# Kernel tuning notes

Measured on AMD Instinct MI355X. Metric: run time of the kernel, lower is better.

Reference implementation:

```python
import jax, jax.numpy as jnp
from jax import lax
import numpy as np

VAR0, VAR1 = 0.1, 0.2
K_TOP, T1, T2 = 5, 0.35, 0.5
ALPHA, GAMMA, BETA = 0.25, 2.0, 0.11


def point_form(b):
    # center form (cx,cy,w,h) -> corner form (x1,y1,x2,y2)
    return jnp.concatenate([b[:, :2] - b[:, 2:] / 2, b[:, :2] + b[:, 2:] / 2], axis=-1)


def jaccard(a, b):
    # a: [N,4], b: [P,4] corner boxes -> IoU [N,P]
    lt = jnp.maximum(a[:, None, :2], b[None, :, :2])
    rb = jnp.minimum(a[:, None, 2:], b[None, :, 2:])
    wh = jnp.clip(rb - lt, 0.0)
    inter = wh[..., 0] * wh[..., 1]
    area_a = ((a[:, 2] - a[:, 0]) * (a[:, 3] - a[:, 1]))[:, None]
    area_b = ((b[:, 2] - b[:, 0]) * (b[:, 3] - b[:, 1]))[None, :]
    return inter / (area_a + area_b - inter)


def encode(matched, priors):
    # matched: corner boxes [P,4], priors: center form [P,4]
    g_cxcy = ((matched[:, :2] + matched[:, 2:]) / 2 - priors[:, :2]) / (VAR0 * priors[:, 2:])
    g_wh = jnp.log((matched[:, 2:] - matched[:, :2]) / priors[:, 2:]) / VAR1
    return jnp.concatenate([g_cxcy, g_wh], axis=-1)


def decode(loc, priors):
    cxcy = priors[:, :2] + loc[:, :2] * VAR0 * priors[:, 2:]
    wh = priors[:, 2:] * jnp.exp(loc[:, 2:] * VAR1)
    return jnp.concatenate([cxcy - wh / 2, cxcy + wh / 2], axis=-1)


def _bce_logits(x, t):
    return jnp.maximum(x, 0.0) - x * t + jnp.log1p(jnp.exp(-jnp.abs(x)))


def focal_loss(logits, target, f_iou=None):
    C = logits.shape[-1]
    t = target.reshape(-1, 1)
    keep = (t >= 0.0).astype(logits.dtype)
    t = jnp.maximum(t, 0.0)
    pos = jnp.sum(t > 0.0).astype(logits.dtype)
    x = jnp.take_along_axis(logits.reshape(-1, C), t.astype(jnp.int32), axis=1)
    ce = _bce_logits(x, t)
    a = t * ALPHA + (1.0 - t) * (1.0 - ALPHA)
    p = jax.nn.sigmoid(x)
    pt = jnp.where(t == 1.0, p, 1.0 - p)
    if f_iou is not None:
        a = lax.stop_gradient(f_iou.reshape(-1, 1)) * a
    loss = a * (1.0 - pt) ** GAMMA * ce * keep
    return jnp.sum(loss) / jnp.maximum(pos, 1.0)


def smoothl1_masked(pred, target, mask):
    # equals SmoothL1Loss on the masked rows: sum(elem)/num_rows
    x = jnp.abs(pred - target)
    elem = jnp.where(x >= BETA, x - 0.5 * BETA, 0.5 * x * x / BETA)
    n = jnp.sum(mask).astype(pred.dtype)
    return jnp.sum(elem * mask[..., None].astype(pred.dtype)) / jnp.maximum(n, 1.0)


def match_image(loc_pred, tgt, priors_c, priors_pt):
    N = tgt.shape[0]
    P = priors_c.shape[0]
    truths = tgt[:, :4]
    labels = tgt[:, 4]
    iou = jaccard(truths, priors_pt)  # [N,P]
    bt_score = jnp.max(iou, axis=0)
    bt_idx = jnp.argmax(iou, axis=0).astype(jnp.int32)

    def greedy(_, st):
        m, s, ix = st
        flat = jnp.argmax(m)
        j = (flat // P).astype(jnp.int32)
        i = (flat % P).astype(jnp.int32)
        v = m.ravel()[flat]
        m = m.at[j, :].set(-1.0)
        m = m.at[:, i].set(-1.0)
        return (m, s.at[i].set(v), ix.at[i].set(j))

    _, bt_score, bt_idx = lax.fori_loop(0, N, greedy, (iou, bt_score, bt_idx))

    conf_s1 = labels[bt_idx]
    conf_s1 = jnp.where(bt_score < T1, 0.0, conf_s1)
    loc_s1 = encode(truths[bt_idx], priors_c)

    decoded = decode(lax.stop_gradient(loc_pred), priors_c)
    c_iou = jaccard(truths, decoded)  # [N,P]
    c_bp_score = jnp.max(c_iou, axis=0)
    c_bp_idx = jnp.argmax(c_iou, axis=0).astype(jnp.int32)
    c_iou = c_iou * (c_iou >= T2).astype(c_iou.dtype)
    tk_s, tk_i = lax.top_k(c_iou, K_TOP)  # per-truth top-K priors
    c_score = jnp.zeros_like(c_bp_score)

    def assign(t, st):
        cbi, cs = st
        i = (t // K_TOP).astype(jnp.int32)
        j = t % K_TOP
        p = tk_i[i, j]
        s = tk_s[i, j]
        cond = (conf_s1[p] < 1.0) & (s > 0.0)
        cbi = cbi.at[p].set(jnp.where(cond, i, cbi[p]))
        cs = cs.at[p].set(jnp.where(cond, s, cs[p]))
        return (cbi, cs)

    c_bp_idx, c_score = lax.fori_loop(0, N * K_TOP, assign, (c_bp_idx, c_score))

    loc_s2 = encode(truths[c_bp_idx], priors_c)
    conf_s2 = labels[c_bp_idx]
    conf_s2 = jnp.where(c_score < T2, -1.0, conf_s2)
    ignore = (bt_score < T1) & (c_bp_score >= T2) & (c_score < T2)
    conf_s1 = jnp.where(ignore, -1.0, conf_s1)
    return conf_s1, loc_s1, conf_s2, loc_s2, c_score


def setup_inputs() -> dict:
    key = jax.random.key(0)
    k1, k2, k3, k4, k5, k6 = jax.random.split(key, 6)
    B, P, N, C = 16, 102400, 32, 2
    loc_data = jax.random.normal(k1, (B, P, 4), jnp.float32)
    conf_data = jax.random.normal(k2, (B, P, C), jnp.float32)
    pcxy = jax.random.uniform(k3, (P, 2), jnp.float32, 0.0, 1.0)
    pwh = jax.random.uniform(k4, (P, 2), jnp.float32, 0.02, 0.25)
    priors = jnp.concatenate([pcxy, pwh], axis=-1)
    tcxy = jax.random.uniform(k5, (B, N, 2), jnp.float32, 0.1, 0.9)
    twh = jax.random.uniform(k6, (B, N, 2), jnp.float32, 0.05, 0.3)
    x1 = jnp.clip(tcxy - twh / 2, 0.0, 1.0)
    x2 = jnp.clip(tcxy + twh / 2, 0.0, 1.0)
    targets = jnp.concatenate([x1, x2, jnp.ones((B, N, 1), jnp.float32)], axis=-1)
    return {"loc_data": loc_data, "conf_data": conf_data, "priors": priors, "targets": targets}


def reference(loc_data, conf_data, priors, targets):
    priors_c = lax.stop_gradient(priors)  # torch uses priors.data
    tgts = lax.stop_gradient(targets)     # torch uses targets[idx].data
    priors_pt = point_form(priors_c)
    conf_t, loc_t, cconf_t, cloc_t, cc_score = jax.vmap(
        lambda lp, tg: match_image(lp, tg, priors_c, priors_pt))(loc_data, tgts)
    m1 = conf_t > 0.0
    m2 = cconf_t > 0.0
    n1 = jnp.sum(m1)
    n2 = jnp.sum(m2)
    l1 = smoothl1_masked(loc_data, loc_t, m1)
    l2 = smoothl1_masked(loc_data, cloc_t, m2)
    f1 = focal_loss(conf_data, conf_t, None)
    f2 = focal_loss(conf_data, cconf_t, cc_score)
    loc_loss = jnp.where(n1 > 0, l1, 0.0) + jnp.where(n2 > 0, l2, 0.0)
    cls_loss = jnp.where(n1 > 0, f1, 0.0) + jnp.where(n2 > 0, f2, 0.0)
    none_ = (n1 == 0) & (n2 == 0)
    return (jnp.where(none_, 1e-4, loc_loss), jnp.where(none_, 1e-4, cls_loss))
```

## Files before the change

kernel.cpp:

```cpp
#include <hip/hip_runtime.h>
#include <cstdint>
#include <cstddef>

#define VAR0_ 0.1f
#define VAR1_ 0.2f
#define KTOP_ 5
#define T1_ 0.35f
#define T2_ 0.5f
#define ALPHA_ 0.25f
#define BETA_ 0.11f
#define BS 256
#define BSK 128
#define NSPLIT 16
#define ILP 4

__device__ __forceinline__ float sl1(float d) {
    float x = fabsf(d);
    return (x >= BETA_) ? (x - 0.5f * BETA_) : (0.5f * x * x / BETA_);
}

__global__ void k_fat1(const float4* __restrict__ loc4, const float4* __restrict__ priors4,
                       const float* __restrict__ targets,
                       float4* __restrict__ recs4,
                       float* __restrict__ cand_v, int* __restrict__ cand_i,
                       int* __restrict__ cand_cnt,
                       float* __restrict__ part_max, int* __restrict__ part_arg,
                       int P, int N, int CAP, int bxPP) {
    int b = blockIdx.y;
    int tid = threadIdx.x;
    if (blockIdx.x < bxPP) {
        int base = blockIdx.x * (BSK * ILP) + tid;
        __shared__ float4 tr4[64];
        __shared__ float trA[64];
        __shared__ float trT[64];
        for (int t = tid; t < N; t += BSK) {
            float x1 = targets[(size_t)(b * N + t) * 5 + 0];
            float y1 = targets[(size_t)(b * N + t) * 5 + 1];
            float x2 = targets[(size_t)(b * N + t) * 5 + 2];
            float y2 = targets[(size_t)(b * N + t) * 5 + 3];
            tr4[t] = make_float4(x1, y1, x2, y2);
            float a = (x2 - x1) * (y2 - y1);
            trA[t] = a;
            trT[t] = a * 0.33330f;
        }
        __syncthreads();
        if (base >= P) return;

        int iv[ILP]; int val[ILP];
        float px1[ILP], py1[ILP], px2[ILP], py2[ILP], pa[ILP];
#pragma unroll
        for (int k = 0; k < ILP; k++) {
            int i = base + k * BSK; iv[k] = i; val[k] = (i < P);
            float4 pr = val[k] ? priors4[i] : make_float4(0.f, 0.f, 1.f, 1.f);
            px1[k] = pr.x - pr.z * 0.5f; py1[k] = pr.y - pr.w * 0.5f;
            px2[k] = pr.x + pr.z * 0.5f; py2[k] = pr.y + pr.w * 0.5f;
            pa[k] = (px2[k] - px1[k]) * (py2[k] - py1[k]);
        }
        float bi[ILP], bu[ILP]; int bn[ILP];
#pragma unroll
        for (int k = 0; k < ILP; k++) { bi[k] = -1.f; bu[k] = 1.f; bn[k] = 0; }
#pragma unroll 2
        for (int n = 0; n < N; n++) {
            float4 t4 = tr4[n];
            float ta = trA[n];
#pragma unroll
            for (int k = 0; k < ILP; k++) {
                float lx = fmaxf(t4.x, px1[k]), ly = fmaxf(t4.y, py1[k]);
                float rx = fminf(t4.z, px2[k]), ry = fminf(t4.w, py2[k]);
                float w = fmaxf(rx - lx, 0.f), h = fmaxf(ry - ly, 0.f);
                float inter = w * h, uni = ta + pa[k] - inter;
                bool bet = inter * bu[k] > bi[k] * uni;
                bi[k] = bet ? inter : bi[k]; bu[k] = bet ? uni : bu[k]; bn[k] = bet ? n : bn[k];
            }
        }
        float bv[ILP];
#pragma unroll
        for (int k = 0; k < ILP; k++) bv[k] = bi[k] / bu[k];

        float dx1[ILP], dy1[ILP], dx2[ILP], dy2[ILP], da[ILP], daC[ILP];
#pragma unroll
        for (int k = 0; k < ILP; k++) {
            float4 pr = val[k] ? priors4[iv[k]] : make_float4(0.f, 0.f, 1.f, 1.f);
            float4 lc = val[k] ? loc4[(size_t)b * P + iv[k]] : make_float4(0.f, 0.f, 0.f, 0.f);
            float dcx = pr.x + lc.x * VAR0_ * pr.z;
            float dcy = pr.y + lc.y * VAR0_ * pr.w;
            float dw = pr.z * expf(lc.z * VAR1_);
            float dh = pr.w * expf(lc.w * VAR1_);
            dx1[k] = dcx - dw * 0.5f; dy1[k] = dcy - dh * 0.5f;
            dx2[k] = dcx + dw * 0.5f; dy2[k] = dcy + dh * 0.5f;
            da[k] = (dx2[k] - dx1[k]) * (dy2[k] - dy1[k]);
            daC[k] = da[k] * 0.33330f;
        }
        unsigned long long hm[ILP];
#pragma unroll
        for (int k = 0; k < ILP; k++) hm[k] = 0ull;
#pragma unroll 2
        for (int n = 0; n < N; n++) {
            float4 t4 = tr4[n];
            float tt = trT[n];
#pragma unroll
            for (int k = 0; k < ILP; k++) {
                float lx = fmaxf(t4.x, dx1[k]), ly = fmaxf(t4.y, dy1[k]);
                float rx = fminf(t4.z, dx2[k]), ry = fminf(t4.w, dy2[k]);
                float w = fmaxf(rx - lx, 0.f), h = fmaxf(ry - ly, 0.f);
                float inter = w * h;
                if (inter >= tt + daC[k]) hm[k] |= (1ull << n);
            }
        }
#pragma unroll
        for (int k = 0; k < ILP; k++) {
            if (!val[k]) continue;
            int had = 0;
            unsigned long long m = hm[k];
            while (m) {
                int n = __ffsll((long long)m) - 1;
                m &= m - 1;
                float4 t4 = tr4[n];
                float lx = fmaxf(t4.x, dx1[k]), ly = fmaxf(t4.y, dy1[k]);
                float rx = fminf(t4.z, dx2[k]), ry = fminf(t4.w, dy2[k]);
                float w = fmaxf(rx - lx, 0.f), h = fmaxf(ry - ly, 0.f);
                float inter = w * h;
                float v = inter / (trA[n] + da[k] - inter);
                if (v >= T2_) {
                    had = 1;
                    int pos = atomicAdd(&cand_cnt[b * N + n], 1);
                    if (pos < CAP) {
                        size_t o = (size_t)(b * N + n) * CAP + pos;
                        cand_v[o] = v; cand_i[o] = iv[k];
                    }
                }
            }
            recs4[(size_t)b * P + iv[k]] =
                make_float4(bv[k], __int_as_float(bn[k] | (had << 16)), __int_as_float(0), 0.f);
        }
    } else {
        int idx = blockIdx.x - bxPP;
        int s = idx % NSPLIT, g = idx / NSPLIT;
        int n0 = g * 4;
        int chunk = (P + NSPLIT - 1) / NSPLIT;
        int i0 = s * chunk;
        int i1 = min(P, i0 + chunk);
        float tx1[4], ty1[4], tx2[4], ty2[4], ta[4];
#pragma unroll
        for (int k = 0; k < 4; k++) {
            int n = min(n0 + k, N - 1);
            tx1[k] = targets[(size_t)(b * N + n) * 5 + 0];
            ty1[k] = targets[(size_t)(b * N + n) * 5 + 1];
            tx2[k] = targets[(size_t)(b * N + n) * 5 + 2];
            ty2[k] = targets[(size_t)(b * N + n) * 5 + 3];
            ta[k] = (tx2[k] - tx1[k]) * (ty2[k] - ty1[k]);
        }
        float cI[4], cU[4]; int cX[4];
#pragma unroll
        for (int k = 0; k < 4; k++) { cI[k] = -1.f; cU[k] = 1.f; cX[k] = 0x7fffffff; }
        for (int i = i0 + tid; i < i1; i += BSK) {
            float4 pr = priors4[i];
            float px1 = pr.x - pr.z * 0.5f, py1 = pr.y - pr.w * 0.5f;
            float px2 = pr.x + pr.z * 0.5f, py2 = pr.y + pr.w * 0.5f;
            float pa = (px2 - px1) * (py2 - py1);
#pragma unroll
            for (int k = 0; k < 4; k++) {
                float lx = fmaxf(tx1[k], px1), ly = fmaxf(ty1[k], py1);
                float rx = fminf(tx2[k], px2), ry = fminf(ty2[k], py2);
                float w = fmaxf(rx - lx, 0.f), h = fmaxf(ry - ly, 0.f);
                float inter = w * h;
                float uni = ta[k] + pa - inter;
                bool bet = inter * cU[k] > cI[k] * uni;
                cI[k] = bet ? inter : cI[k]; cU[k] = bet ? uni : cU[k]; cX[k] = bet ? i : cX[k];
            }
        }
        int lane = tid & 63, wid = tid >> 6;
        __shared__ float swv[BSK / 64];
        __shared__ int swi[BSK / 64];
#pragma unroll
        for (int k = 0; k < 4; k++) {
            if (n0 + k >= N) break;
            float bv = cI[k] / cU[k];
            int bx = cX[k];
#pragma unroll
            for (int off = 32; off > 0; off >>= 1) {
                float ov = __shfl_xor(bv, off);
                int oi = __shfl_xor(bx, off);
                if (ov > bv || (ov == bv && oi < bx)) { bv = ov; bx = oi; }
            }
            if (lane == 0) { swv[wid] = bv; swi[wid] = bx; }
            __syncthreads();
            if (tid == 0) {
                float fv = swv[0]; int fi = swi[0];
                for (int wv = 1; wv < BSK / 64; wv++) {
                    if (swv[wv] > fv || (swv[wv] == fv && swi[wv] < fi)) { fv = swv[wv]; fi = swi[wv]; }
                }
                int o = (b * N + (n0 + k)) * NSPLIT + s;
                part_max[o] = fv; part_arg[o] = fi;
            }
            __syncthreads();
        }
    }
}

__global__ void k_fat2(const float4* __restrict__ loc4, const float4* __restrict__ priors4,
                       const float* __restrict__ targets,
                       const float* __restrict__ cand_v, const int* __restrict__ cand_i,
                       const int* __restrict__ cand_cnt,
                       float* __restrict__ tk_s, int* __restrict__ tk_i,
                       const float* __restrict__ part_max, const int* __restrict__ part_arg,
                       float* __restrict__ recs,
                       int P, int N, int CAP) {
    int b = blockIdx.y;
    int tid = threadIdx.x;
    if ((int)blockIdx.x < N) {
        int n = blockIdx.x;
        int row = b * N + n;
        float vals[KTOP_]; int ids[KTOP_];
#pragma unroll
        for (int k = 0; k < KTOP_; k++) { vals[k] = -1.f; ids[k] = 0x7fffffff; }
        int cnt = cand_cnt[row];
        if (cnt <= CAP) {
            for (int k = tid; k < cnt; k += blockDim.x) {
                float cv = cand_v[(size_t)row * CAP + k];
                int ci = cand_i[(size_t)row * CAP + k];
#pragma unroll
                for (int q = 0; q < KTOP_; q++) {
                    bool better = (cv > vals[q]) || ((cv == vals[q]) && (ci < ids[q]));
                    float tv = better ? cv : vals[q]; int ti = better ? ci : ids[q];
                    cv = better ? vals[q] : cv; ci = better ? ids[q] : ci;
                    vals[q] = tv; ids[q] = ti;
                }
            }
        } else {
            float tx1 = targets[(size_t)row * 5 + 0], ty1 = targets[(size_t)row * 5 + 1];
            float tx2 = targets[(size_t)row * 5 + 2], ty2 = targets[(size_t)row * 5 + 3];
            float ta = (tx2 - tx1) * (ty2 - ty1);
            for (int i = tid; i < P; i += blockDim.x) {
                float4 pr = priors4[i];
                size_t bp = (size_t)b * P + i;
                float4 lc = loc4[bp];
                float dcx = pr.x + lc.x * VAR0_ * pr.z;
                float dcy = pr.y + lc.y * VAR0_ * pr.w;
                float dw = pr.z * expf(lc.z * VAR1_);
                float dh = pr.w * expf(lc.w * VAR1_);
                float dx1 = dcx - dw * 0.5f, dy1 = dcy - dh * 0.5f;
                float dx2 = dcx + dw * 0.5f, dy2 = dcy + dh * 0.5f;
                float lx = fmaxf(tx1, dx1), ly = fmaxf(ty1, dy1);
                float rx = fminf(tx2, dx2), ry = fminf(ty2, dy2);
                float w = fmaxf(rx - lx, 0.f), h = fmaxf(ry - ly, 0.f);
                float inter = w * h;
                float uni = ta + (dx2 - dx1) * (dy2 - dy1) - inter;
                if (inter >= uni * 0.4999990f) {
                    float v = inter / uni;
                    if (v >= T2_) {
                        float cv = v; int ci = i;
#pragma unroll
                        for (int q = 0; q < KTOP_; q++) {
                            bool better = (cv > vals[q]) || ((cv == vals[q]) && (ci < ids[q]));
                            float tv = better ? cv : vals[q]; int ti = better ? ci : ids[q];
                            cv = better ? vals[q] : cv; ci = better ? ids[q] : ci;
                            vals[q] = tv; ids[q] = ti;
                        }
                    }
                }
            }
        }
        __shared__ float mv[BS * KTOP_];
        __shared__ int mi[BS * KTOP_];
#pragma unroll
        for (int k = 0; k < KTOP_; k++) { mv[tid * KTOP_ + k] = vals[k]; mi[tid * KTOP_ + k] = ids[k]; }
        __syncthreads();
        for (int s = BS / 2; s > 0; s >>= 1) {
            if (tid < s) {
#pragma unroll
                for (int j = 0; j < KTOP_; j++) {
                    float cv = mv[(tid + s) * KTOP_ + j];
                    int ci = mi[(tid + s) * KTOP_ + j];
#pragma unroll
                    for (int q = 0; q < KTOP_; q++) {
                        bool better = (cv > vals[q]) || ((cv == vals[q]) && (ci < ids[q]));
                        float tv = better ? cv : vals[q]; int ti = better ? ci : ids[q];
                        cv = better ? vals[q] : cv; ci = better ? ids[q] : ci;
                        vals[q] = tv; ids[q] = ti;
                    }
                }
#pragma unroll
                for (int k = 0; k < KTOP_; k++) { mv[tid * KTOP_ + k] = vals[k]; mi[tid * KTOP_ + k] = ids[k]; }
            }
            __syncthreads();
        }
        if (tid == 0) {
#pragma unroll
            for (int k = 0; k < KTOP_; k++) {
                tk_s[(size_t)row * KTOP_ + k] = (vals[k] > 0.f) ? vals[k] : 0.f;
                tk_i[(size_t)row * KTOP_ + k] = (ids[k] == 0x7fffffff) ? 0 : ids[k];
            }
        }
    } else {
        int lane = tid & 63, wid = tid >> 6;
        extern __shared__ unsigned int mask[];
        int maskWords = (P + 31) >> 5;
        for (int w = tid; w < maskWords; w += BS) mask[w] = 0u;

        float rmax = -2.f; int rarg = 0x7fffffff; int alive = 0;
        float tx1 = 0.f, ty1 = 0.f, tx2 = 0.f, ty2 = 0.f, ta = 0.f;
        if (wid == 0 && lane < N) {
            float bv = -2.f; int bi = 0x7fffffff;
            for (int s = 0; s < NSPLIT; s++) {
                int o = (b * N + lane) * NSPLIT + s;
                float v = part_max[o]; int ix = part_arg[o];
                if (v > bv || (v == bv && ix < bi)) { bv = v; bi = ix; }
            }
            rmax = bv; rarg = bi;
            alive = 1;
            tx1 = targets[(size_t)(b * N + lane) * 5 + 0];
            ty1 = targets[(size_t)(b * N + lane) * 5 + 1];
            tx2 = targets[(size_t)(b * N + lane) * 5 + 2];
            ty2 = targets[(size_t)(b * N + lane) * 5 + 3];
            ta = (tx2 - tx1) * (ty2 - ty1);
        }
        __syncthreads();

        for (int it = 0; it < N; it++) {
            int sel = 0;
            if (wid == 0) {
                float v = (lane < N && alive) ? rmax : -3.f;
                int idx = lane;
#pragma unroll
                for (int off = 32; off > 0; off >>= 1) {
                    float ov = __shfl_xor(v, off);
                    int oi = __shfl_xor(idx, off);
                    if (ov > v || (ov == v && oi < idx)) { v = ov; idx = oi; }
                }
                int bj = idx;
                float bv = v;
                sel = __shfl(rarg, bj);
                if (lane == bj) alive = 0;
                if (lane == 0) {
                    float* base = recs + 4 * ((size_t)b * P + sel);
                    int wrd = __float_as_int(base[1]);
                    base[0] = bv;
                    base[1] = __int_as_float((wrd & ~0xFFFF) | bj);
                    mask[sel >> 5] |= (1u << (sel & 31));
                }
            }
            __syncthreads();
            if (wid == 0) {
                unsigned long long coll = __ballot(lane < N && alive && rarg == sel);
                while (coll) {
                    int r = __ffsll((long long)coll) - 1;
                    coll &= coll - 1;
                    float rx1 = __shfl(tx1, r), ry1 = __shfl(ty1, r);
                    float rx2 = __shfl(tx2, r), ry2 = __shfl(ty2, r);
                    float ra = __shfl(ta, r);
                    float n_i = -2.f, n_u = 1.f; int ni = 0x7fffffff;
                    for (int i = lane; i < P; i += 64) {
                        if (mask[i >> 5] & (1u << (i & 31))) continue;
                        float4 pr = priors4[i];
                        float px1 = pr.x - pr.z * 0.5f, py1 = pr.y - pr.w * 0.5f;
                        float px2 = pr.x + pr.z * 0.5f, py2 = pr.y + pr.w * 0.5f;
                        float lx = fmaxf(rx1, px1), ly = fmaxf(ry1, py1);
                        float rx = fminf(rx2, px2), ry = fminf(ry2, py2);
                        float w = fmaxf(rx - lx, 0.f), h = fmaxf(ry - ly, 0.f);
                        float inter = w * h;
                        float uni = ra + (px2 - px1) * (py2 - py1) - inter;
                        bool better = inter * n_u > n_i * uni;
                        n_i = better ? inter : n_i; n_u = better ? uni : n_u; ni = better ? i : ni;
                    }
                    float nv = n_i / n_u;
#pragma unroll
                    for (int off = 32; off > 0; off >>= 1) {
                        float ov = __shfl_xor(nv, off);
                        int oi = __shfl_xor(ni, off);
                        if (ov > nv || (ov == nv && oi < ni)) { nv = ov; ni = oi; }
                    }
                    if (lane == r) { rmax = nv; rarg = ni; }
                }
            }
            __syncthreads();
        }
    }
}

__global__ void k_assign(const float* __restrict__ targets,
                         const float* __restrict__ tk_s, const int* __restrict__ tk_i,
                         float* __restrict__ recs, int P, int N) {
    int b = blockIdx.x;
    int tid = threadIdx.x;
    int T = N * KTOP_;
    __shared__ int sh_p[512];
    __shared__ float sh_s[512];
    __shared__ int sh_c[512];
    if (tid < T) {
        int i = tid / KTOP_, j = tid % KTOP_;
        int p = tk_i[(size_t)(b * N + i) * KTOP_ + j];
        float s = tk_s[(size_t)(b * N + i) * KTOP_ + j];
        const float* base = recs + 4 * ((size_t)b * P + p);
        float bs = base[0];
        int bj = __float_as_int(base[1]) & 0xFFFF;
        float conf1 = (bs < T1_) ? 0.f : targets[(size_t)(b * N + bj) * 5 + 4];
        sh_p[tid] = p; sh_s[tid] = s;
        sh_c[tid] = (conf1 < 1.f && s > 0.f) ? 1 : 0;
    }
    __syncthreads();
    if (tid < T && sh_c[tid]) {
        int p = sh_p[tid];
        bool last = true;
        for (int t2 = tid + 1; t2 < T; t2++) {
            if (sh_c[t2] && sh_p[t2] == p) { last = false; break; }
        }
        if (last) {
            float* base = recs + 4 * ((size_t)b * P + p);
            base[2] = __int_as_float(tid / KTOP_);
            base[3] = sh_s[tid];
        }
    }
}

__global__ void k_loss(const float4* __restrict__ loc4, const float* __restrict__ conf,
                       const float4* __restrict__ priors4, const float* __restrict__ targets,
                       const float4* __restrict__ recs4,
                       double* __restrict__ partials,
                       int P, int N, int C) {
    int b = blockIdx.y;
    int i = blockIdx.x * blockDim.x + threadIdx.x;
    double l1 = 0.0, l2 = 0.0, f1 = 0.0, f2 = 0.0;
    int n1 = 0, n2 = 0;
    if (i < P) {
        size_t bp = (size_t)b * P + i;
        float4 r = recs4[bp];
        float bs = r.x;
        int widx = __float_as_int(r.y);
        int bj = widx & 0xFFFF;
        int hadCand = (widx >> 16) & 1;
        float cs = r.w;
        int cj = (cs > 0.f) ? __float_as_int(r.z) : 0;
        float lab1 = targets[(size_t)(b * N + bj) * 5 + 4];
        float conf1 = (bs < T1_) ? 0.f : lab1;
        if ((bs < T1_) && hadCand && (cs < T2_)) conf1 = -1.f;
        float lab2 = targets[(size_t)(b * N + cj) * 5 + 4];
        float conf2 = (cs < T2_) ? -1.f : lab2;
        bool m1 = conf1 > 0.f, m2 = conf2 > 0.f;
        n1 = m1 ? 1 : 0; n2 = m2 ? 1 : 0;

        if (m1 || m2) {
            float4 pr = priors4[i];
            float pcx = pr.x, pcy = pr.y, pw = pr.z, ph = pr.w;
            float4 lc = loc4[bp];
            float p0 = lc.x, p1 = lc.y, p2 = lc.z, p3 = lc.w;
            if (m1) {
                const float* tb = &targets[(size_t)(b * N + bj) * 5];
                float gx = ((tb[0] + tb[2]) * 0.5f - pcx) / (VAR0_ * pw);
                float gy = ((tb[1] + tb[3]) * 0.5f - pcy) / (VAR0_ * ph);
                float gw = logf((tb[2] - tb[0]) / pw) / VAR1_;
                float gh = logf((tb[3] - tb[1]) / ph) / VAR1_;
                l1 = (double)(sl1(p0 - gx) + sl1(p1 - gy) + sl1(p2 - gw) + sl1(p3 - gh));
            }
            if (m2) {
                const float* tb = &targets[(size_t)(b * N + cj) * 5];
                float gx = ((tb[0] + tb[2]) * 0.5f - pcx) / (VAR0_ * pw);
                float gy = ((tb[1] + tb[3]) * 0.5f - pcy) / (VAR0_ * ph);
                float gw = logf((tb[2] - tb[0]) / pw) / VAR1_;
                float gh = logf((tb[3] - tb[1]) / ph) / VAR1_;
                l2 = (double)(sl1(p0 - gx) + sl1(p1 - gy) + sl1(p2 - gw) + sl1(p3 - gh));
            }
        }
        float x0, x1v;
        if (C == 2) {
            float2 cv2 = ((const float2*)conf)[bp];
            x0 = cv2.x; x1v = cv2.y;
        } else {
            x0 = conf[bp * C + 0]; x1v = conf[bp * C + 1];
        }
        {
            float t = fmaxf(conf1, 0.f);
            float keep = (conf1 >= 0.f) ? 1.f : 0.f;
            float x = (t >= 1.f) ? x1v : x0;
            float ce = fmaxf(x, 0.f) - x * t + log1pf(expf(-fabsf(x)));
            float a = t * ALPHA_ + (1.f - t) * (1.f - ALPHA_);
            float pr_ = 1.f / (1.f + expf(-x));
            float pt = (t == 1.f) ? pr_ : (1.f - pr_);
            float om = 1.f - pt;
            f1 = (double)(a * om * om * ce * keep);
        }
        {
            float t = fmaxf(conf2, 0.f);
            float keep = (conf2 >= 0.f) ? 1.f : 0.f;
            float x = (t >= 1.f) ? x1v : x0;
            float ce = fmaxf(x, 0.f) - x * t + log1pf(expf(-fabsf(x)));
            float a = cs * (t * ALPHA_ + (1.f - t) * (1.f - ALPHA_));
            float pr_ = 1.f / (1.f + expf(-x));
            float pt = (t == 1.f) ? pr_ : (1.f - pr_);
            float om = 1.f - pt;
            f2 = (double)(a * om * om * ce * keep);
        }
    }
    int tid = threadIdx.x;
    int lane = tid & 63, wid = tid >> 6;
#pragma unroll
    for (int off = 32; off > 0; off >>= 1) {
        l1 += __shfl_xor(l1, off);
        l2 += __shfl_xor(l2, off);
        f1 += __shfl_xor(f1, off);
        f2 += __shfl_xor(f2, off);
        n1 += __shfl_xor(n1, off);
        n2 += __shfl_xor(n2, off);
    }
    __shared__ double swd[BS / 64][4];
    __shared__ int swn[BS / 64][2];
    if (lane == 0) {
        swd[wid][0] = l1; swd[wid][1] = l2; swd[wid][2] = f1; swd[wid][3] = f2;
        swn[wid][0] = n1; swn[wid][1] = n2;
    }
    __syncthreads();
    if (tid == 0) {
        double a0 = 0, a1 = 0, a2 = 0, a3 = 0; int b0 = 0, b1 = 0;
        for (int wv = 0; wv < BS / 64; wv++) {
            a0 += swd[wv][0]; a1 += swd[wv][1]; a2 += swd[wv][2]; a3 += swd[wv][3];
            b0 += swn[wv][0]; b1 += swn[wv][1];
        }
        int blk = blockIdx.y * gridDim.x + blockIdx.x;
        partials[(size_t)blk * 6 + 0] = a0;
        partials[(size_t)blk * 6 + 1] = a1;
        partials[(size_t)blk * 6 + 2] = a2;
        partials[(size_t)blk * 6 + 3] = a3;
        partials[(size_t)blk * 6 + 4] = (double)b0;
        partials[(size_t)blk * 6 + 5] = (double)b1;
    }
}

__global__ void k_final(const double* __restrict__ partials, int nPart, float* __restrict__ out) {
    int tid = threadIdx.x;
    double a[6] = {0, 0, 0, 0, 0, 0};
    for (int k = tid; k < nPart; k += BS) {
#pragma unroll
        for (int j = 0; j < 6; j++) a[j] += partials[(size_t)k * 6 + j];
    }
    __shared__ double sd[BS * 6];
#pragma unroll
    for (int j = 0; j < 6; j++) sd[tid * 6 + j] = a[j];
    __syncthreads();
    for (int s = BS / 2; s > 0; s >>= 1) {
        if (tid < s) {
#pragma unroll
            for (int j = 0; j < 6; j++) sd[tid * 6 + j] += sd[(tid + s) * 6 + j];
        }
        __syncthreads();
    }
    if (tid == 0) {
        double L1 = sd[0], L2 = sd[1], F1 = sd[2], F2 = sd[3], N1 = sd[4], N2 = sd[5];
        double l1v = L1 / fmax(N1, 1.0), l2v = L2 / fmax(N2, 1.0);
        double f1v = F1 / fmax(N1, 1.0), f2v = F2 / fmax(N2, 1.0);
        double locl = (N1 > 0 ? l1v : 0.0) + (N2 > 0 ? l2v : 0.0);
        double clsl = (N1 > 0 ? f1v : 0.0) + (N2 > 0 ? f2v : 0.0);
        if (N1 == 0 && N2 == 0) { locl = 1e-4; clsl = 1e-4; }
        out[0] = (float)locl;
        out[1] = (float)clsl;
    }
}

extern "C" void kernel_launch(void* const* d_in, const int* in_sizes, int n_in,
                              void* d_out, int out_size, void* d_ws, size_t ws_size,
                              hipStream_t stream) {
    const float* targets = (const float*)d_in[3];
    const float* conf = (const float*)d_in[1];
    const float4* loc4 = (const float4*)d_in[0];
    const float4* priors4 = (const float4*)d_in[2];

    int P = in_sizes[2] / 4;
    int B = in_sizes[0] / (P * 4);
    int N = in_sizes[3] / (B * 5);
    int C = in_sizes[1] / (B * P);
    const int CAP = 2048;
    size_t BP = (size_t)B * P;

    unsigned char* ws = (unsigned char*)d_ws;
    size_t off = 0;
    auto alloc = [&](size_t bytes) { size_t cur = off; off += (bytes + 255) & ~(size_t)255; return cur; };
    float* recs = (float*)(ws + alloc(BP * 16));
    float* part_max = (float*)(ws + alloc((size_t)B * N * NSPLIT * 4));
    int* part_arg = (int*)(ws + alloc((size_t)B * N * NSPLIT * 4));
    float* tk_s = (float*)(ws + alloc((size_t)B * N * KTOP_ * 4));
    int* tk_i = (int*)(ws + alloc((size_t)B * N * KTOP_ * 4));
    float* cand_v = (float*)(ws + alloc((size_t)B * N * CAP * 4));
    int* cand_i = (int*)(ws + alloc((size_t)B * N * CAP * 4));
    int* cand_cnt = (int*)(ws + alloc((size_t)B * N * 4));
    int bx = (P + BS - 1) / BS;
    double* partials = (double*)(ws + alloc((size_t)bx * B * 6 * 8));
    float* out = (float*)d_out;

    hipMemsetAsync(cand_cnt, 0, (size_t)B * N * 4, stream);

    int bxPP = (P + BSK * ILP - 1) / (BSK * ILP);
    int ngroup = (N + 3) / 4;
    int bxRM = NSPLIT * ngroup;
    k_fat1<<<dim3(bxPP + bxRM, B), BSK, 0, stream>>>(loc4, priors4, targets, (float4*)recs,
                                                     cand_v, cand_i, cand_cnt,
                                                     part_max, part_arg, P, N, CAP, bxPP);

    int maskWords = (P + 31) / 32;
    size_t shmem = (size_t)maskWords * 4;
    k_fat2<<<dim3(N + 1, B), BS, shmem, stream>>>(loc4, priors4, targets,
                                                  cand_v, cand_i, cand_cnt, tk_s, tk_i,
                                                  part_max, part_arg, recs, P, N, CAP);

    k_assign<<<dim3(B), BS, 0, stream>>>(targets, tk_s, tk_i, recs, P, N);
    k_loss<<<dim3(bx, B), BS, 0, stream>>>(loc4, conf, priors4, targets, (const float4*)recs,
                                           partials, P, N, C);
    k_final<<<1, BS, 0, stream>>>(partials, bx * B, out);
}
```

Baseline: 213.6 us.

## Split fused match kernel in two and fold final reduction into loss kernel

The per-prior matching work and the per-target row-max partial work, previously packed into one launch by branching on block index, become two separate kernels, and the row-max kernel now runs with 256-thread blocks instead of 128. The final reduction kernel is removed: the last loss block, detected through an atomic completion counter that is zeroed with the existing memset, performs the global sum and writes the output. This saves one launch and drops branch divergence between block roles. In exchange it adds a separate launch for the row-max work, which no longer runs concurrently with the per-prior work, and adds a threadfence/atomic handshake.

```diff
diff --git a/kernel.cpp b/kernel.cpp
--- a/kernel.cpp
+++ b/kernel.cpp
@@ -19,182 +19,184 @@
     return (x >= BETA_) ? (x - 0.5f * BETA_) : (0.5f * x * x / BETA_);
 }
 
-__global__ void k_fat1(const float4* __restrict__ loc4, const float4* __restrict__ priors4,
-                       const float* __restrict__ targets,
-                       float4* __restrict__ recs4,
-                       float* __restrict__ cand_v, int* __restrict__ cand_i,
-                       int* __restrict__ cand_cnt,
-                       float* __restrict__ part_max, int* __restrict__ part_arg,
-                       int P, int N, int CAP, int bxPP) {
+__global__ void k_per_prior(const float4* __restrict__ loc4, const float4* __restrict__ priors4,
+                            const float* __restrict__ targets,
+                            float4* __restrict__ recs4,
+                            float* __restrict__ cand_v, int* __restrict__ cand_i,
+                            int* __restrict__ cand_cnt,
+                            int P, int N, int CAP) {
     int b = blockIdx.y;
     int tid = threadIdx.x;
-    if (blockIdx.x < bxPP) {
-        int base = blockIdx.x * (BSK * ILP) + tid;
-        __shared__ float4 tr4[64];
-        __shared__ float trA[64];
-        __shared__ float trT[64];
-        for (int t = tid; t < N; t += BSK) {
-            float x1 = targets[(size_t)(b * N + t) * 5 + 0];
-            float y1 = targets[(size_t)(b * N + t) * 5 + 1];
-            float x2 = targets[(size_t)(b * N + t) * 5 + 2];
-            float y2 = targets[(size_t)(b * N + t) * 5 + 3];
-            tr4[t] = make_float4(x1, y1, x2, y2);
-            float a = (x2 - x1) * (y2 - y1);
-            trA[t] = a;
-            trT[t] = a * 0.33330f;
-        }
+    int base = blockIdx.x * (BSK * ILP) + tid;
+    __shared__ float4 tr4[64];
+    __shared__ float trA[64];
+    __shared__ float trT[64];
+    for (int t = tid; t < N; t += BSK) {
+        float x1 = targets[(size_t)(b * N + t) * 5 + 0];
+        float y1 = targets[(size_t)(b * N + t) * 5 + 1];
+        float x2 = targets[(size_t)(b * N + t) * 5 + 2];
+        float y2 = targets[(size_t)(b * N + t) * 5 + 3];
+        tr4[t] = make_float4(x1, y1, x2, y2);
+        float a = (x2 - x1) * (y2 - y1);
+        trA[t] = a;
+        trT[t] = a * 0.33330f;
+    }
+    __syncthreads();
+    if (base >= P) return;
+
+    int iv[ILP]; int val[ILP];
+    float px1[ILP], py1[ILP], px2[ILP], py2[ILP], pa[ILP];
+#pragma unroll
+    for (int k = 0; k < ILP; k++) {
+        int i = base + k * BSK; iv[k] = i; val[k] = (i < P);
+        float4 pr = val[k] ? priors4[i] : make_float4(0.f, 0.f, 1.f, 1.f);
+        px1[k] = pr.x - pr.z * 0.5f; py1[k] = pr.y - pr.w * 0.5f;
+        px2[k] = pr.x + pr.z * 0.5f; py2[k] = pr.y + pr.w * 0.5f;
+        pa[k] = (px2[k] - px1[k]) * (py2[k] - py1[k]);
+    }
+
+    float bi[ILP], bu[ILP]; int bn[ILP];
+#pragma unroll
+    for (int k = 0; k < ILP; k++) { bi[k] = -1.f; bu[k] = 1.f; bn[k] = 0; }
+#pragma unroll 2
+    for (int n = 0; n < N; n++) {
+        float4 t4 = tr4[n];
+        float ta = trA[n];
+#pragma unroll
+        for (int k = 0; k < ILP; k++) {
+            float lx = fmaxf(t4.x, px1[k]), ly = fmaxf(t4.y, py1[k]);
+            float rx = fminf(t4.z, px2[k]), ry = fminf(t4.w, py2[k]);
+            float w = fmaxf(rx - lx, 0.f), h = fmaxf(ry - ly, 0.f);
+            float inter = w * h, uni = ta + pa[k] - inter;
+            bool bet = inter * bu[k] > bi[k] * uni;
+            bi[k] = bet ? inter : bi[k]; bu[k] = bet ? uni : bu[k]; bn[k] = bet ? n : bn[k];
+        }
+    }
+    float bv[ILP];
+#pragma unroll
+    for (int k = 0; k < ILP; k++) bv[k] = bi[k] / bu[k];
+
+    float dx1[ILP], dy1[ILP], dx2[ILP], dy2[ILP], da[ILP], daC[ILP];
+#pragma unroll
+    for (int k = 0; k < ILP; k++) {
+        float4 pr = val[k] ? priors4[iv[k]] : make_float4(0.f, 0.f, 1.f, 1.f);
+        float4 lc = val[k] ? loc4[(size_t)b * P + iv[k]] : make_float4(0.f, 0.f, 0.f, 0.f);
+        float dcx = pr.x + lc.x * VAR0_ * pr.z;
+        float dcy = pr.y + lc.y * VAR0_ * pr.w;
+        float dw = pr.z * expf(lc.z * VAR1_);
+        float dh = pr.w * expf(lc.w * VAR1_);
+        dx1[k] = dcx - dw * 0.5f; dy1[k] = dcy - dh * 0.5f;
+        dx2[k] = dcx + dw * 0.5f; dy2[k] = dcy + dh * 0.5f;
+        da[k] = (dx2[k] - dx1[k]) * (dy2[k] - dy1[k]);
+        daC[k] = da[k] * 0.33330f;
+    }
+    unsigned long long hm[ILP];
+#pragma unroll
+    for (int k = 0; k < ILP; k++) hm[k] = 0ull;
+#pragma unroll 2
+    for (int n = 0; n < N; n++) {
+        float4 t4 = tr4[n];
+        float tt = trT[n];
+#pragma unroll
+        for (int k = 0; k < ILP; k++) {
+            float lx = fmaxf(t4.x, dx1[k]), ly = fmaxf(t4.y, dy1[k]);
+            float rx = fminf(t4.z, dx2[k]), ry = fminf(t4.w, dy2[k]);
+            float w = fmaxf(rx - lx, 0.f), h = fmaxf(ry - ly, 0.f);
+            float inter = w * h;
+            if (inter >= tt + daC[k]) hm[k] |= (1ull << n);
+        }
+    }
+#pragma unroll
+    for (int k = 0; k < ILP; k++) {
+        if (!val[k]) continue;
+        int had = 0;
+        unsigned long long m = hm[k];
+        while (m) {
+            int n = __ffsll((long long)m) - 1;
+            m &= m - 1;
+            float4 t4 = tr4[n];
+            float lx = fmaxf(t4.x, dx1[k]), ly = fmaxf(t4.y, dy1[k]);
+            float rx = fminf(t4.z, dx2[k]), ry = fminf(t4.w, dy2[k]);
+            float w = fmaxf(rx - lx, 0.f), h = fmaxf(ry - ly, 0.f);
+            float inter = w * h;
+            float v = inter / (trA[n] + da[k] - inter);
+            if (v >= T2_) {
+                had = 1;
+                int pos = atomicAdd(&cand_cnt[b * N + n], 1);
+                if (pos < CAP) {
+                    size_t o = (size_t)(b * N + n) * CAP + pos;
+                    cand_v[o] = v; cand_i[o] = iv[k];
+                }
+            }
+        }
+        recs4[(size_t)b * P + iv[k]] =
+            make_float4(bv[k], __int_as_float(bn[k] | (had << 16)), __int_as_float(0), 0.f);
+    }
+}
+
+__global__ void k_row_max_part(const float4* __restrict__ priors4, const float* __restrict__ targets,
+                               float* __restrict__ part_max, int* __restrict__ part_arg,
+                               int P, int N) {
+    int s = blockIdx.x, b = blockIdx.y, g = blockIdx.z;
+    int n0 = g * 4;
+    int chunk = (P + NSPLIT - 1) / NSPLIT;
+    int i0 = s * chunk;
+    int i1 = min(P, i0 + chunk);
+    float tx1[4], ty1[4], tx2[4], ty2[4], ta[4];
+#pragma unroll
+    for (int k = 0; k < 4; k++) {
+        int n = min(n0 + k, N - 1);
+        tx1[k] = targets[(size_t)(b * N + n) * 5 + 0];
+        ty1[k] = targets[(size_t)(b * N + n) * 5 + 1];
+        tx2[k] = targets[(size_t)(b * N + n) * 5 + 2];
+        ty2[k] = targets[(size_t)(b * N + n) * 5 + 3];
+        ta[k] = (tx2[k] - tx1[k]) * (ty2[k] - ty1[k]);
+    }
+    float cI[4], cU[4]; int cX[4];
+#pragma unroll
+    for (int k = 0; k < 4; k++) { cI[k] = -1.f; cU[k] = 1.f; cX[k] = 0x7fffffff; }
+    for (int i = i0 + threadIdx.x; i < i1; i += BS) {
+        float4 pr = priors4[i];
+        float px1 = pr.x - pr.z * 0.5f, py1 = pr.y - pr.w * 0.5f;
+        float px2 = pr.x + pr.z * 0.5f, py2 = pr.y + pr.w * 0.5f;
+        float pa = (px2 - px1) * (py2 - py1);
+#pragma unroll
+        for (int k = 0; k < 4; k++) {
+            float lx = fmaxf(tx1[k], px1), ly = fmaxf(ty1[k], py1);
+            float rx = fminf(tx2[k], px2), ry = fminf(ty2[k], py2);
+            float w = fmaxf(rx - lx, 0.f), h = fmaxf(ry - ly, 0.f);
+            float inter = w * h;
+            float uni = ta[k] + pa - inter;
+            bool bet = inter * cU[k] > cI[k] * uni;
+            cI[k] = bet ? inter : cI[k]; cU[k] = bet ? uni : cU[k]; cX[k] = bet ? i : cX[k];
+        }
+    }
+    int tid = threadIdx.x;
+    int lane = tid & 63, wid = tid >> 6;
+    __shared__ float swv[BS / 64];
+    __shared__ int swi[BS / 64];
+#pragma unroll
+    for (int k = 0; k < 4; k++) {
+        if (n0 + k >= N) break;
+        float bv = cI[k] / cU[k];
+        int bx = cX[k];
+#pragma unroll
+        for (int off = 32; off > 0; off >>= 1) {
+            float ov = __shfl_xor(bv, off);
+            int oi = __shfl_xor(bx, off);
+            if (ov > bv || (ov == bv && oi < bx)) { bv = ov; bx = oi; }
+        }
+        if (lane == 0) { swv[wid] = bv; swi[wid] = bx; }
         __syncthreads();
-        if (base >= P) return;
-
-        int iv[ILP]; int val[ILP];
-        float px1[ILP], py1[ILP], px2[ILP], py2[ILP], pa[ILP];
-#pragma unroll
-        for (int k = 0; k < ILP; k++) {
-            int i = base + k * BSK; iv[k] = i; val[k] = (i < P);
-            float4 pr = val[k] ? priors4[i] : make_float4(0.f, 0.f, 1.f, 1.f);
-            px1[k] = pr.x - pr.z * 0.5f; py1[k] = pr.y - pr.w * 0.5f;
-            px2[k] = pr.x + pr.z * 0.5f; py2[k] = pr.y + pr.w * 0.5f;
-            pa[k] = (px2[k] - px1[k]) * (py2[k] - py1[k]);
-        }
-        float bi[ILP], bu[ILP]; int bn[ILP];
-#pragma unroll
-        for (int k = 0; k < ILP; k++) { bi[k] = -1.f; bu[k] = 1.f; bn[k] = 0; }
-#pragma unroll 2
-        for (int n = 0; n < N; n++) {
-            float4 t4 = tr4[n];
-            float ta = trA[n];
-#pragma unroll
-            for (int k = 0; k < ILP; k++) {
-                float lx = fmaxf(t4.x, px1[k]), ly = fmaxf(t4.y, py1[k]);
-                float rx = fminf(t4.z, px2[k]), ry = fminf(t4.w, py2[k]);
-                float w = fmaxf(rx - lx, 0.f), h = fmaxf(ry - ly, 0.f);
-                float inter = w * h, uni = ta + pa[k] - inter;
-                bool bet = inter * bu[k] > bi[k] * uni;
-                bi[k] = bet ? inter : bi[k]; bu[k] = bet ? uni : bu[k]; bn[k] = bet ? n : bn[k];
-            }
-        }
-        float bv[ILP];
-#pragma unroll
-        for (int k = 0; k < ILP; k++) bv[k] = bi[k] / bu[k];
-
-        float dx1[ILP], dy1[ILP], dx2[ILP], dy2[ILP], da[ILP], daC[ILP];
-#pragma unroll
-        for (int k = 0; k < ILP; k++) {
-            float4 pr = val[k] ? priors4[iv[k]] : make_float4(0.f, 0.f, 1.f, 1.f);
-            float4 lc = val[k] ? loc4[(size_t)b * P + iv[k]] : make_float4(0.f, 0.f, 0.f, 0.f);
-            float dcx = pr.x + lc.x * VAR0_ * pr.z;
-            float dcy = pr.y + lc.y * VAR0_ * pr.w;
-            float dw = pr.z * expf(lc.z * VAR1_);
-            float dh = pr.w * expf(lc.w * VAR1_);
-            dx1[k] = dcx - dw * 0.5f; dy1[k] = dcy - dh * 0.5f;
-            dx2[k] = dcx + dw * 0.5f; dy2[k] = dcy + dh * 0.5f;
-            da[k] = (dx2[k] - dx1[k]) * (dy2[k] - dy1[k]);
-            daC[k] = da[k] * 0.33330f;
-        }
-        unsigned long long hm[ILP];
-#pragma unroll
-        for (int k = 0; k < ILP; k++) hm[k] = 0ull;
-#pragma unroll 2
-        for (int n = 0; n < N; n++) {
-            float4 t4 = tr4[n];
-            float tt = trT[n];
-#pragma unroll
-            for (int k = 0; k < ILP; k++) {
-                float lx = fmaxf(t4.x, dx1[k]), ly = fmaxf(t4.y, dy1[k]);
-                float rx = fminf(t4.z, dx2[k]), ry = fminf(t4.w, dy2[k]);
-                float w = fmaxf(rx - lx, 0.f), h = fmaxf(ry - ly, 0.f);
-                float inter = w * h;
-                if (inter >= tt + daC[k]) hm[k] |= (1ull << n);
-            }
-        }
-#pragma unroll
-        for (int k = 0; k < ILP; k++) {
-            if (!val[k]) continue;
-            int had = 0;
-            unsigned long long m = hm[k];
-            while (m) {
-                int n = __ffsll((long long)m) - 1;
-                m &= m - 1;
-                float4 t4 = tr4[n];
-                float lx = fmaxf(t4.x, dx1[k]), ly = fmaxf(t4.y, dy1[k]);
-                float rx = fminf(t4.z, dx2[k]), ry = fminf(t4.w, dy2[k]);
-                float w = fmaxf(rx - lx, 0.f), h = fmaxf(ry - ly, 0.f);
-                float inter = w * h;
-                float v = inter / (trA[n] + da[k] - inter);
-                if (v >= T2_) {
-                    had = 1;
-                    int pos = atomicAdd(&cand_cnt[b * N + n], 1);
-                    if (pos < CAP) {
-                        size_t o = (size_t)(b * N + n) * CAP + pos;
-                        cand_v[o] = v; cand_i[o] = iv[k];
-                    }
-                }
-            }
-            recs4[(size_t)b * P + iv[k]] =
-                make_float4(bv[k], __int_as_float(bn[k] | (had << 16)), __int_as_float(0), 0.f);
-        }
-    } else {
-        int idx = blockIdx.x - bxPP;
-        int s = idx % NSPLIT, g = idx / NSPLIT;
-        int n0 = g * 4;
-        int chunk = (P + NSPLIT - 1) / NSPLIT;
-        int i0 = s * chunk;
-        int i1 = min(P, i0 + chunk);
-        float tx1[4], ty1[4], tx2[4], ty2[4], ta[4];
-#pragma unroll
-        for (int k = 0; k < 4; k++) {
-            int n = min(n0 + k, N - 1);
-            tx1[k] = targets[(size_t)(b * N + n) * 5 + 0];
-            ty1[k] = targets[(size_t)(b * N + n) * 5 + 1];
-            tx2[k] = targets[(size_t)(b * N + n) * 5 + 2];
-            ty2[k] = targets[(size_t)(b * N + n) * 5 + 3];
-            ta[k] = (tx2[k] - tx1[k]) * (ty2[k] - ty1[k]);
-        }
-        float cI[4], cU[4]; int cX[4];
-#pragma unroll
-        for (int k = 0; k < 4; k++) { cI[k] = -1.f; cU[k] = 1.f; cX[k] = 0x7fffffff; }
-        for (int i = i0 + tid; i < i1; i += BSK) {
-            float4 pr = priors4[i];
-            float px1 = pr.x - pr.z * 0.5f, py1 = pr.y - pr.w * 0.5f;
-            float px2 = pr.x + pr.z * 0.5f, py2 = pr.y + pr.w * 0.5f;
-            float pa = (px2 - px1) * (py2 - py1);
-#pragma unroll
-            for (int k = 0; k < 4; k++) {
-                float lx = fmaxf(tx1[k], px1), ly = fmaxf(ty1[k], py1);
-                float rx = fminf(tx2[k], px2), ry = fminf(ty2[k], py2);
-                float w = fmaxf(rx - lx, 0.f), h = fmaxf(ry - ly, 0.f);
-                float inter = w * h;
-                float uni = ta[k] + pa - inter;
-                bool bet = inter * cU[k] > cI[k] * uni;
-                cI[k] = bet ? inter : cI[k]; cU[k] = bet ? uni : cU[k]; cX[k] = bet ? i : cX[k];
-            }
-        }
-        int lane = tid & 63, wid = tid >> 6;
-        __shared__ float swv[BSK / 64];
-        __shared__ int swi[BSK / 64];
-#pragma unroll
-        for (int k = 0; k < 4; k++) {
-            if (n0 + k >= N) break;
-            float bv = cI[k] / cU[k];
-            int bx = cX[k];
-#pragma unroll
-            for (int off = 32; off > 0; off >>= 1) {
-                float ov = __shfl_xor(bv, off);
-                int oi = __shfl_xor(bx, off);
-                if (ov > bv || (ov == bv && oi < bx)) { bv = ov; bx = oi; }
-            }
-            if (lane == 0) { swv[wid] = bv; swi[wid] = bx; }
-            __syncthreads();
-            if (tid == 0) {
-                float fv = swv[0]; int fi = swi[0];
-                for (int wv = 1; wv < BSK / 64; wv++) {
-                    if (swv[wv] > fv || (swv[wv] == fv && swi[wv] < fi)) { fv = swv[wv]; fi = swi[wv]; }
-                }
-                int o = (b * N + (n0 + k)) * NSPLIT + s;
-                part_max[o] = fv; part_arg[o] = fi;
-            }
-            __syncthreads();
-        }
+        if (tid == 0) {
+            float fv = swv[0]; int fi = swi[0];
+            for (int wv = 1; wv < BS / 64; wv++) {
+                if (swv[wv] > fv || (swv[wv] == fv && swi[wv] < fi)) { fv = swv[wv]; fi = swi[wv]; }
+            }
+            int o = (b * N + (n0 + k)) * NSPLIT + s;
+            part_max[o] = fv; part_arg[o] = fi;
+        }
+        __syncthreads();
     }
 }
 
@@ -413,11 +415,12 @@
     }
 }
 
-__global__ void k_loss(const float4* __restrict__ loc4, const float* __restrict__ conf,
-                       const float4* __restrict__ priors4, const float* __restrict__ targets,
-                       const float4* __restrict__ recs4,
-                       double* __restrict__ partials,
-                       int P, int N, int C) {
+__global__ void k_loss_final(const float4* __restrict__ loc4, const float* __restrict__ conf,
+                             const float4* __restrict__ priors4, const float* __restrict__ targets,
+                             const float4* __restrict__ recs4,
+                             double* __restrict__ partials, int* __restrict__ done_cnt,
+                             float* __restrict__ out,
+                             int P, int N, int C, int nPart) {
     int b = blockIdx.y;
     int i = blockIdx.x * blockDim.x + threadIdx.x;
     double l1 = 0.0, l2 = 0.0, f1 = 0.0, f2 = 0.0;
@@ -438,7 +441,6 @@
         float conf2 = (cs < T2_) ? -1.f : lab2;
         bool m1 = conf1 > 0.f, m2 = conf2 > 0.f;
         n1 = m1 ? 1 : 0; n2 = m2 ? 1 : 0;
-
         if (m1 || m2) {
             float4 pr = priors4[i];
             float pcx = pr.x, pcy = pr.y, pw = pr.z, ph = pr.w;
@@ -509,6 +511,7 @@
         swn[wid][0] = n1; swn[wid][1] = n2;
     }
     __syncthreads();
+    __shared__ int s_last;
     if (tid == 0) {
         double a0 = 0, a1 = 0, a2 = 0, a3 = 0; int b0 = 0, b1 = 0;
         for (int wv = 0; wv < BS / 64; wv++) {
@@ -522,36 +525,39 @@
         partials[(size_t)blk * 6 + 3] = a3;
         partials[(size_t)blk * 6 + 4] = (double)b0;
         partials[(size_t)blk * 6 + 5] = (double)b1;
-    }
-}
-
-__global__ void k_final(const double* __restrict__ partials, int nPart, float* __restrict__ out) {
-    int tid = threadIdx.x;
-    double a[6] = {0, 0, 0, 0, 0, 0};
-    for (int k = tid; k < nPart; k += BS) {
-#pragma unroll
-        for (int j = 0; j < 6; j++) a[j] += partials[(size_t)k * 6 + j];
-    }
-    __shared__ double sd[BS * 6];
-#pragma unroll
-    for (int j = 0; j < 6; j++) sd[tid * 6 + j] = a[j];
+        __threadfence();
+        int prev = atomicAdd(done_cnt, 1);
+        s_last = (prev == nPart - 1) ? 1 : 0;
+    }
     __syncthreads();
-    for (int s = BS / 2; s > 0; s >>= 1) {
-        if (tid < s) {
-#pragma unroll
-            for (int j = 0; j < 6; j++) sd[tid * 6 + j] += sd[(tid + s) * 6 + j];
-        }
+    if (s_last) {
+        __threadfence();
+        double a[6] = {0, 0, 0, 0, 0, 0};
+        for (int k = tid; k < nPart; k += BS) {
+#pragma unroll
+            for (int j = 0; j < 6; j++) a[j] += partials[(size_t)k * 6 + j];
+        }
+        __shared__ double sd[BS * 6];
+#pragma unroll
+        for (int j = 0; j < 6; j++) sd[tid * 6 + j] = a[j];
         __syncthreads();
-    }
-    if (tid == 0) {
-        double L1 = sd[0], L2 = sd[1], F1 = sd[2], F2 = sd[3], N1 = sd[4], N2 = sd[5];
-        double l1v = L1 / fmax(N1, 1.0), l2v = L2 / fmax(N2, 1.0);
-        double f1v = F1 / fmax(N1, 1.0), f2v = F2 / fmax(N2, 1.0);
-        double locl = (N1 > 0 ? l1v : 0.0) + (N2 > 0 ? l2v : 0.0);
-        double clsl = (N1 > 0 ? f1v : 0.0) + (N2 > 0 ? f2v : 0.0);
-        if (N1 == 0 && N2 == 0) { locl = 1e-4; clsl = 1e-4; }
-        out[0] = (float)locl;
-        out[1] = (float)clsl;
+        for (int s = BS / 2; s > 0; s >>= 1) {
+            if (tid < s) {
+#pragma unroll
+                for (int j = 0; j < 6; j++) sd[tid * 6 + j] += sd[(tid + s) * 6 + j];
+            }
+            __syncthreads();
+        }
+        if (tid == 0) {
+            double L1 = sd[0], L2 = sd[1], F1 = sd[2], F2 = sd[3], N1 = sd[4], N2 = sd[5];
+            double l1v = L1 / fmax(N1, 1.0), l2v = L2 / fmax(N2, 1.0);
+            double f1v = F1 / fmax(N1, 1.0), f2v = F2 / fmax(N2, 1.0);
+            double locl = (N1 > 0 ? l1v : 0.0) + (N2 > 0 ? l2v : 0.0);
+            double clsl = (N1 > 0 ? f1v : 0.0) + (N2 > 0 ? f2v : 0.0);
+            if (N1 == 0 && N2 == 0) { locl = 1e-4; clsl = 1e-4; }
+            out[0] = (float)locl;
+            out[1] = (float)clsl;
+        }
     }
 }
 
@@ -580,28 +586,27 @@
     int* tk_i = (int*)(ws + alloc((size_t)B * N * KTOP_ * 4));
     float* cand_v = (float*)(ws + alloc((size_t)B * N * CAP * 4));
     int* cand_i = (int*)(ws + alloc((size_t)B * N * CAP * 4));
-    int* cand_cnt = (int*)(ws + alloc((size_t)B * N * 4));
+    int* cand_cnt = (int*)(ws + alloc(((size_t)B * N + 1) * 4));
     int bx = (P + BS - 1) / BS;
     double* partials = (double*)(ws + alloc((size_t)bx * B * 6 * 8));
     float* out = (float*)d_out;
-
-    hipMemsetAsync(cand_cnt, 0, (size_t)B * N * 4, stream);
-
-    int bxPP = (P + BSK * ILP - 1) / (BSK * ILP);
+    int* done_cnt = cand_cnt + B * N;
+
+    hipMemsetAsync(cand_cnt, 0, ((size_t)B * N + 1) * 4, stream);
+
+    int bx4 = (P + BSK * ILP - 1) / (BSK * ILP);
+    k_per_prior<<<dim3(bx4, B), BSK, 0, stream>>>(loc4, priors4, targets, (float4*)recs,
+                                                  cand_v, cand_i, cand_cnt, P, N, CAP);
     int ngroup = (N + 3) / 4;
-    int bxRM = NSPLIT * ngroup;
-    k_fat1<<<dim3(bxPP + bxRM, B), BSK, 0, stream>>>(loc4, priors4, targets, (float4*)recs,
-                                                     cand_v, cand_i, cand_cnt,
-                                                     part_max, part_arg, P, N, CAP, bxPP);
-
+    k_row_max_part<<<dim3(NSPLIT, B, ngroup), BS, 0, stream>>>(priors4, targets,
+                                                               part_max, part_arg, P, N);
     int maskWords = (P + 31) / 32;
     size_t shmem = (size_t)maskWords * 4;
     k_fat2<<<dim3(N + 1, B), BS, shmem, stream>>>(loc4, priors4, targets,
                                                   cand_v, cand_i, cand_cnt, tk_s, tk_i,
                                                   part_max, part_arg, recs, P, N, CAP);
-
     k_assign<<<dim3(B), BS, 0, stream>>>(targets, tk_s, tk_i, recs, P, N);
-    k_loss<<<dim3(bx, B), BS, 0, stream>>>(loc4, conf, priors4, targets, (const float4*)recs,
-                                           partials, P, N, C);
-    k_final<<<1, BS, 0, stream>>>(partials, bx * B, out);
+    k_loss_final<<<dim3(bx, B), BS, 0, stream>>>(loc4, conf, priors4, targets,
+                                                 (const float4*)recs, partials, done_cnt,
+                                                 out, P, N, C, bx * B);
 }
```

Result: slower. 321.6 us (+50.6%).
